# Kernel optimization log

Measured on AMD Instinct MI355X. Metric: run time of the kernel, lower is better.

## Reference

```python
import jax, jax.numpy as jnp
import numpy as np

T, H = 4096, 7168          # tokens, hidden size
Q_LORA, KV_LORA = 1536, 512
ROPE, NOPE, NH = 64, 128, 16
QK = NOPE + ROPE
MAXPOS, SLOTS = 8192, 16384
EPS = 1e-6


def _build_cos_sin_cache():
    # rotary cache layout used by the module: [max_pos, rope] = cos_half || sin_half
    half = ROPE // 2
    inv_freq = 1.0 / (10000.0 ** (np.arange(0, half, dtype=np.float32) / half))
    t = np.arange(MAXPOS, dtype=np.float32)
    freqs = np.outer(t, inv_freq)  # [MAXPOS, half]
    return jnp.asarray(np.concatenate([np.cos(freqs), np.sin(freqs)], axis=-1))


def setup_inputs() -> dict:
    key = jax.random.key(0)
    ks = jax.random.split(key, 8)
    return {
        "hidden_states": jax.random.normal(ks[0], (T, H), jnp.float32),
        "positions": jax.random.randint(ks[1], (T,), 0, MAXPOS, jnp.int32),
        "w_qkv_a": jax.random.normal(ks[2], (H, Q_LORA + KV_LORA + ROPE), jnp.float32) * 0.02,
        "q_a_ln_w": jnp.ones((Q_LORA,), jnp.float32),
        "w_q_b": jax.random.normal(ks[3], (Q_LORA, NH * QK), jnp.float32) * 0.02,
        "kv_a_ln_w": jnp.ones((KV_LORA,), jnp.float32),
        "w_kc": jax.random.normal(ks[4], (NH, NOPE, KV_LORA), jnp.float32) * 0.02,
        "cos_sin_cache": _build_cos_sin_cache(),
        "k_cache": jnp.zeros((SLOTS, KV_LORA), jnp.float32),
        "rope_cache": jnp.zeros((SLOTS, ROPE), jnp.float32),
        "slot_mapping": jnp.arange(T, dtype=jnp.int32),
    }


def _rms_norm(x, w, eps=EPS):
    return x * jax.lax.rsqrt(jnp.mean(x * x, axis=-1, keepdims=True) + eps) * w


def _interleave_rope(x, cos, sin):
    # npu_interleave_rope: de-interleave even/odd lanes into halves, then
    # apply neox-style rotation with full-dim (repeated) cos/sin.
    x1 = x[..., 0::2]
    x2 = x[..., 1::2]
    rot = jnp.concatenate([x1, x2], axis=-1)
    h = rot.shape[-1] // 2
    rot_half = jnp.concatenate([-rot[..., h:], rot[..., :h]], axis=-1)
    return rot * cos + rot_half * sin


def reference(hidden_states, positions, w_qkv_a, q_a_ln_w, w_q_b, kv_a_ln_w,
              w_kc, cos_sin_cache, k_cache, rope_cache, slot_mapping):
    # get_sin_cos: gather cache, chunk in halves, repeat each to full rope dim
    cs = cos_sin_cache[positions]                 # [T, ROPE]
    cos, sin = jnp.split(cs, 2, axis=-1)          # [T, ROPE/2] each
    cos = jnp.tile(cos, (1, 2))                   # [T, ROPE]
    sin = jnp.tile(sin, (1, 2))

    # fused qkv_a projection -> q low-rank + latent kv cache
    qkv = hidden_states @ w_qkv_a                 # [T, Q_LORA + KV_LORA + ROPE]
    q_low = qkv[:, :Q_LORA]
    latent = qkv[:, Q_LORA:]

    # q path: RMSNorm -> q_b projection -> per-head split
    q = _rms_norm(q_low, q_a_ln_w)
    q = (q @ w_q_b).reshape(-1, NH, QK)           # [T, NH, QK]
    q_nope, q_pe = q[..., :NOPE], q[..., NOPE:]

    # absorb: q_nope @ w_kc per head -> [T, NH, KV_LORA]
    q_nope = jnp.einsum("thn,hnk->thk", q_nope, w_kc)
    # interleaved rope on q_pe
    q_pe = _interleave_rope(q_pe, cos[:, None, :], sin[:, None, :])

    # kv path (npu_kv_rmsnorm_rope_cache): rmsnorm latent, rope the rope part,
    # scatter both into the paged caches at slot_mapping
    k_nope = _rms_norm(latent[:, :KV_LORA], kv_a_ln_w)     # [T, KV_LORA]
    k_rope = _interleave_rope(latent[:, KV_LORA:], cos, sin)  # [T, ROPE]
    k_cache = k_cache.at[slot_mapping].set(k_nope)
    rope_cache = rope_cache.at[slot_mapping].set(k_rope)

    q_out = jnp.concatenate([q_nope, q_pe], axis=-1)       # [T, NH, KV_LORA+ROPE]
    k_out = jnp.concatenate([k_nope, k_rope], axis=-1)     # [T, KV_LORA+ROPE]
    return q_out, k_out, k_cache, rope_cache
```

## Files before the change

kernel.cpp:

```cpp
#include <hip/hip_runtime.h>
#include <hip/hip_bf16.h>

typedef __bf16 bf16_t;
typedef __bf16 bf16x8 __attribute__((ext_vector_type(8)));
typedef float f32x4 __attribute__((ext_vector_type(4)));
typedef unsigned int uint;

#define T_TOK 4096
#define H_DIM 7168
#define QLORA 1536
#define KVLORA 512
#define ROPE_D 64
#define NOPE_D 128
#define NHEAD 16
#define NQKV 2112
#define NQB  3072
#define EPS_F 1e-6f


__global__ void cast_f32_bf16(const float* __restrict__ in, bf16_t* __restrict__ out, long n8)
{
    long stride = (long)gridDim.x * blockDim.x;
    for (long i = (long)blockIdx.x * blockDim.x + threadIdx.x; i < n8; i += stride) {
        const float4 a = ((const float4*)in)[i * 2];
        const float4 b = ((const float4*)in)[i * 2 + 1];
        bf16x8 v;
        v[0] = (bf16_t)a.x; v[1] = (bf16_t)a.y; v[2] = (bf16_t)a.z; v[3] = (bf16_t)a.w;
        v[4] = (bf16_t)b.x; v[5] = (bf16_t)b.y; v[6] = (bf16_t)b.z; v[7] = (bf16_t)b.w;
        ((bf16x8*)out)[i] = v;
    }
}

__global__ __launch_bounds__(256) void transpose_cast(const float* __restrict__ in,
                                                      bf16_t* __restrict__ out, int R, int C)
{
    __shared__ float tile[32][33];
    const int bx = blockIdx.x * 32;
    const int by = blockIdx.y * 32;
    const int tx = threadIdx.x & 31, ty = threadIdx.x >> 5;
    #pragma unroll
    for (int r = ty; r < 32; r += 8)
        tile[r][tx] = in[(long)(by + r) * C + bx + tx];
    __syncthreads();
    #pragma unroll
    for (int r = ty; r < 32; r += 8)
        out[(long)(bx + r) * R + by + tx] = (bf16_t)tile[tx][r];
}

__device__ inline float block_sum_256(float v)
{
    #pragma unroll
    for (int off = 32; off > 0; off >>= 1) v += __shfl_xor(v, off, 64);
    __shared__ float tmp[4];
    __syncthreads();
    if ((threadIdx.x & 63) == 0) tmp[threadIdx.x >> 6] = v;
    __syncthreads();
    return tmp[0] + tmp[1] + tmp[2] + tmp[3];
}

__global__ __launch_bounds__(256) void rmsq_kside_kernel(
    const float* __restrict__ qkv, const float* __restrict__ qkvB,
    const float* __restrict__ q_w, const float* __restrict__ kv_w,
    const float* __restrict__ cos_sin, const int* __restrict__ positions,
    const int* __restrict__ slot_map,
    bf16_t* __restrict__ q_a, float* __restrict__ k_out,
    float* __restrict__ kc_out, float* __restrict__ rc_out)
{
    const int t = blockIdx.x;
    const float* x = qkv + (long)t * NQKV;
    const float* xB = qkvB ? qkvB + (long)t * NQKV : nullptr;

    float loc[6];
    float ss = 0.f;
    #pragma unroll
    for (int i = 0; i < 6; i++) {
        int idx = threadIdx.x + 256 * i;
        float v = x[idx];
        if (xB) v += xB[idx];
        loc[i] = v; ss += v * v;
    }
    ss = block_sum_256(ss);
    const float scq = rsqrtf(ss / (float)QLORA + EPS_F);
    #pragma unroll
    for (int i = 0; i < 6; i++) {
        int idx = threadIdx.x + 256 * i;
        q_a[(long)t * QLORA + idx] = (bf16_t)(loc[i] * scq * q_w[idx]);
    }

    const float* lat = x + QLORA;
    const float* latB = xB ? xB + QLORA : nullptr;
    float v0 = lat[threadIdx.x];
    float v1 = lat[threadIdx.x + 256];
    if (latB) { v0 += latB[threadIdx.x]; v1 += latB[threadIdx.x + 256]; }
    float ssk = v0 * v0 + v1 * v1;
    ssk = block_sum_256(ssk);
    const float sck = rsqrtf(ssk / (float)KVLORA + EPS_F);
    const int slot = slot_map[t];
    const float a0 = v0 * sck * kv_w[threadIdx.x];
    const float a1 = v1 * sck * kv_w[threadIdx.x + 256];
    k_out[(long)t * 576 + threadIdx.x]        = a0;
    k_out[(long)t * 576 + 256 + threadIdx.x]  = a1;
    kc_out[(long)slot * KVLORA + threadIdx.x]       = a0;
    kc_out[(long)slot * KVLORA + 256 + threadIdx.x] = a1;
    if (threadIdx.x < 32) {
        const int j = threadIdx.x;
        const int pos = positions[t];
        const float c = cos_sin[pos * 64 + j];
        const float s = cos_sin[pos * 64 + 32 + j];
        float x1 = lat[KVLORA + 2 * j];
        float x2 = lat[KVLORA + 2 * j + 1];
        if (latB) { x1 += latB[KVLORA + 2 * j]; x2 += latB[KVLORA + 2 * j + 1]; }
        const float o1 = x1 * c - x2 * s;
        const float o2 = x2 * c + x1 * s;
        k_out[(long)t * 576 + 512 + j]      = o1;
        k_out[(long)t * 576 + 512 + 32 + j] = o2;
        rc_out[(long)slot * 64 + j]      = o1;
        rc_out[(long)slot * 64 + 32 + j] = o2;
    }
}

#define GBM 128
#define GBN 128
#define GBK 64

__global__ __launch_bounds__(512) void gemm_mfma(
    const bf16_t* __restrict__ A, int lda, long sA,
    const bf16_t* __restrict__ Bt, int ldb, long sB,
    float* __restrict__ C, int ldc, long sC,
    int K, int N)
{
    __shared__ bf16_t As[2][GBM * GBK];
    __shared__ bf16_t Bs[2][GBN * GBK];

    const int nwg = gridDim.x * gridDim.y;
    const int bid = blockIdx.y * gridDim.x + blockIdx.x;
    const int cpx = nwg >> 3;
    const int swz = (bid & 7) * cpx + (bid >> 3);
    const int bx = swz % gridDim.x;
    const int by = swz / gridDim.x;

    const int tid = threadIdx.x;
    const int lane = tid & 63;
    const int w = tid >> 6;
    const int wr = w >> 2, wc = w & 3;
    const int fr = lane & 15;
    const int kg = lane >> 4;

    const long brow = (long)by * GBM;
    const long bcol = (long)bx * GBN;

    const bf16_t* Ab = A + blockIdx.z * sA + brow * lda;
    const bf16_t* Bb = Bt + blockIdx.z * sB;
    float* Cb = C + blockIdx.z * sC + brow * ldc;

    const int srow = w * 16 + (lane >> 3);
    const int scol = (((lane & 7) ^ (lane >> 3)) * 8);

    const uint rd_sw = (uint)((kg * 16) ^ ((fr & 7) << 4));
    const uint a_base = (uint)(uintptr_t)(&As[0][0]) + (uint)((wr * 64 + fr) * 128) + rd_sw;
    const uint b_base = (uint)(uintptr_t)(&Bs[0][0]) + (uint)((wc * 32 + fr) * 128) + rd_sw;

    f32x4 acc[4][2] = {};

    const int nt = K / GBK;

    auto stage = [&](int buf, int k0) {
        #pragma unroll
        for (int it = 0; it < 2; it++) {
            const int r = srow + it * 8;
            __builtin_amdgcn_global_load_lds(
                (const __attribute__((address_space(1))) void*)(Ab + (long)r * lda + k0 + scol),
                (__attribute__((address_space(3))) void*)(&As[buf][(w * 16 + it * 8) * GBK]),
                16, 0, 0);
        }
        #pragma unroll
        for (int it = 0; it < 2; it++) {
            const int r = srow + it * 8;
            long bn = bcol + r; if (bn >= N) bn = N - 1;
            __builtin_amdgcn_global_load_lds(
                (const __attribute__((address_space(1))) void*)(Bb + bn * ldb + k0 + scol),
                (__attribute__((address_space(3))) void*)(&Bs[buf][(w * 16 + it * 8) * GBK]),
                16, 0, 0);
        }
    };

    stage(0, 0);
    asm volatile("s_waitcnt vmcnt(0)" ::: "memory");
    __builtin_amdgcn_s_barrier();

    int cur = 0;
    for (int t = 0; t < nt; ++t) {
        if (t + 1 < nt) stage(cur ^ 1, (t + 1) * GBK);

        const uint aa  = a_base + (uint)(cur * (GBM * GBK * 2));
        const uint bb  = b_base + (uint)(cur * (GBN * GBK * 2));
        const uint aaX = aa ^ 64u;
        const uint bbX = bb ^ 64u;
        bf16x8 a00, a01, a02, a03, a10, a11, a12, a13, b00, b01, b10, b11;
        asm volatile("ds_read_b128 %0, %1 offset:0"    : "=v"(a00) : "v"(aa));
        asm volatile("ds_read_b128 %0, %1 offset:2048" : "=v"(a01) : "v"(aa));
        asm volatile("ds_read_b128 %0, %1 offset:4096" : "=v"(a02) : "v"(aa));
        asm volatile("ds_read_b128 %0, %1 offset:6144" : "=v"(a03) : "v"(aa));
        asm volatile("ds_read_b128 %0, %1 offset:0"    : "=v"(a10) : "v"(aaX));
        asm volatile("ds_read_b128 %0, %1 offset:2048" : "=v"(a11) : "v"(aaX));
        asm volatile("ds_read_b128 %0, %1 offset:4096" : "=v"(a12) : "v"(aaX));
        asm volatile("ds_read_b128 %0, %1 offset:6144" : "=v"(a13) : "v"(aaX));
        asm volatile("ds_read_b128 %0, %1 offset:0"    : "=v"(b00) : "v"(bb));
        asm volatile("ds_read_b128 %0, %1 offset:2048" : "=v"(b01) : "v"(bb));
        asm volatile("ds_read_b128 %0, %1 offset:0"    : "=v"(b10) : "v"(bbX));
        asm volatile("ds_read_b128 %0, %1 offset:2048" : "=v"(b11) : "v"(bbX));
        asm volatile("s_waitcnt lgkmcnt(0)" ::: "memory");
        __builtin_amdgcn_sched_barrier(0);

        acc[0][0] = __builtin_amdgcn_mfma_f32_16x16x32_bf16(a00, b00, acc[0][0], 0, 0, 0);
        acc[0][1] = __builtin_amdgcn_mfma_f32_16x16x32_bf16(a00, b01, acc[0][1], 0, 0, 0);
        acc[1][0] = __builtin_amdgcn_mfma_f32_16x16x32_bf16(a01, b00, acc[1][0], 0, 0, 0);
        acc[1][1] = __builtin_amdgcn_mfma_f32_16x16x32_bf16(a01, b01, acc[1][1], 0, 0, 0);
        acc[2][0] = __builtin_amdgcn_mfma_f32_16x16x32_bf16(a02, b00, acc[2][0], 0, 0, 0);
        acc[2][1] = __builtin_amdgcn_mfma_f32_16x16x32_bf16(a02, b01, acc[2][1], 0, 0, 0);
        acc[3][0] = __builtin_amdgcn_mfma_f32_16x16x32_bf16(a03, b00, acc[3][0], 0, 0, 0);
        acc[3][1] = __builtin_amdgcn_mfma_f32_16x16x32_bf16(a03, b01, acc[3][1], 0, 0, 0);
        acc[0][0] = __builtin_amdgcn_mfma_f32_16x16x32_bf16(a10, b10, acc[0][0], 0, 0, 0);
        acc[0][1] = __builtin_amdgcn_mfma_f32_16x16x32_bf16(a10, b11, acc[0][1], 0, 0, 0);
        acc[1][0] = __builtin_amdgcn_mfma_f32_16x16x32_bf16(a11, b10, acc[1][0], 0, 0, 0);
        acc[1][1] = __builtin_amdgcn_mfma_f32_16x16x32_bf16(a11, b11, acc[1][1], 0, 0, 0);
        acc[2][0] = __builtin_amdgcn_mfma_f32_16x16x32_bf16(a12, b10, acc[2][0], 0, 0, 0);
        acc[2][1] = __builtin_amdgcn_mfma_f32_16x16x32_bf16(a12, b11, acc[2][1], 0, 0, 0);
        acc[3][0] = __builtin_amdgcn_mfma_f32_16x16x32_bf16(a13, b10, acc[3][0], 0, 0, 0);
        acc[3][1] = __builtin_amdgcn_mfma_f32_16x16x32_bf16(a13, b11, acc[3][1], 0, 0, 0);

        asm volatile("s_waitcnt vmcnt(0)" ::: "memory");
        __builtin_amdgcn_s_barrier();
        cur ^= 1;
    }

    #pragma unroll
    for (int i = 0; i < 4; i++) {
        #pragma unroll
        for (int j = 0; j < 2; j++) {
            const int row0 = wr * 64 + i * 16 + kg * 4;
            const long col = bcol + wc * 32 + j * 16 + fr;
            if (col < N) {
                #pragma unroll
                for (int r = 0; r < 4; r++)
                    Cb[(long)(row0 + r) * ldc + col] = acc[i][j][r];
            }
        }
    }
}

__global__ __launch_bounds__(512) void gemm2_fused(
    const bf16_t* __restrict__ A,
    const bf16_t* __restrict__ Bt,
    const float* __restrict__ cos_sin,
    const int* __restrict__ positions,
    bf16_t* __restrict__ q_nope,
    float* __restrict__ q_out)
{
    __shared__ bf16_t As[2][GBM * GBK];
    __shared__ bf16_t Bs[2][GBN * GBK];

    const int nwg = gridDim.x * gridDim.y;
    const int bid = blockIdx.y * gridDim.x + blockIdx.x;
    const int cpx = nwg >> 3;
    const int swz = (bid & 7) * cpx + (bid >> 3);
    const int bx = swz % gridDim.x;
    const int by = swz / gridDim.x;

    const int tid = threadIdx.x;
    const int lane = tid & 63;
    const int w = tid >> 6;
    const int wr = w >> 2, wc = w & 3;
    const int fr = lane & 15;
    const int kg = lane >> 4;

    const int brow = by * GBM;
    const int bcol = bx * GBN;

    const bf16_t* Ab = A + (long)brow * QLORA;
    const bf16_t* Bb = Bt + (long)bcol * QLORA;

    const int srow = w * 16 + (lane >> 3);
    const int scol = (((lane & 7) ^ (lane >> 3)) * 8);

    const uint rd_sw = (uint)((kg * 16) ^ ((fr & 7) << 4));
    const uint a_base = (uint)(uintptr_t)(&As[0][0]) + (uint)((wr * 64 + fr) * 128) + rd_sw;
    const uint b_base = (uint)(uintptr_t)(&Bs[0][0]) + (uint)((wc * 32 + fr) * 128) + rd_sw;

    f32x4 acc[4][2] = {};

    const int nt = QLORA / GBK;

    auto stage = [&](int buf, int k0) {
        #pragma unroll
        for (int it = 0; it < 2; it++) {
            const int r = srow + it * 8;
            __builtin_amdgcn_global_load_lds(
                (const __attribute__((address_space(1))) void*)(Ab + (long)r * QLORA + k0 + scol),
                (__attribute__((address_space(3))) void*)(&As[buf][(w * 16 + it * 8) * GBK]),
                16, 0, 0);
            __builtin_amdgcn_global_load_lds(
                (const __attribute__((address_space(1))) void*)(Bb + (long)r * QLORA + k0 + scol),
                (__attribute__((address_space(3))) void*)(&Bs[buf][(w * 16 + it * 8) * GBK]),
                16, 0, 0);
        }
    };

    stage(0, 0);
    asm volatile("s_waitcnt vmcnt(0)" ::: "memory");
    __builtin_amdgcn_s_barrier();

    int cur = 0;
    for (int t = 0; t < nt; ++t) {
        if (t + 1 < nt) stage(cur ^ 1, (t + 1) * GBK);

        const uint aa  = a_base + (uint)(cur * (GBM * GBK * 2));
        const uint bb  = b_base + (uint)(cur * (GBN * GBK * 2));
        const uint aaX = aa ^ 64u;
        const uint bbX = bb ^ 64u;
        bf16x8 a00, a01, a02, a03, a10, a11, a12, a13, b00, b01, b10, b11;
        asm volatile("ds_read_b128 %0, %1 offset:0"    : "=v"(a00) : "v"(aa));
        asm volatile("ds_read_b128 %0, %1 offset:2048" : "=v"(a01) : "v"(aa));
        asm volatile("ds_read_b128 %0, %1 offset:4096" : "=v"(a02) : "v"(aa));
        asm volatile("ds_read_b128 %0, %1 offset:6144" : "=v"(a03) : "v"(aa));
        asm volatile("ds_read_b128 %0, %1 offset:0"    : "=v"(a10) : "v"(aaX));
        asm volatile("ds_read_b128 %0, %1 offset:2048" : "=v"(a11) : "v"(aaX));
        asm volatile("ds_read_b128 %0, %1 offset:4096" : "=v"(a12) : "v"(aaX));
        asm volatile("ds_read_b128 %0, %1 offset:6144" : "=v"(a13) : "v"(aaX));
        asm volatile("ds_read_b128 %0, %1 offset:0"    : "=v"(b00) : "v"(bb));
        asm volatile("ds_read_b128 %0, %1 offset:2048" : "=v"(b01) : "v"(bb));
        asm volatile("ds_read_b128 %0, %1 offset:0"    : "=v"(b10) : "v"(bbX));
        asm volatile("ds_read_b128 %0, %1 offset:2048" : "=v"(b11) : "v"(bbX));
        asm volatile("s_waitcnt lgkmcnt(0)" ::: "memory");
        __builtin_amdgcn_sched_barrier(0);

        acc[0][0] = __builtin_amdgcn_mfma_f32_16x16x32_bf16(a00, b00, acc[0][0], 0, 0, 0);
        acc[0][1] = __builtin_amdgcn_mfma_f32_16x16x32_bf16(a00, b01, acc[0][1], 0, 0, 0);
        acc[1][0] = __builtin_amdgcn_mfma_f32_16x16x32_bf16(a01, b00, acc[1][0], 0, 0, 0);
        acc[1][1] = __builtin_amdgcn_mfma_f32_16x16x32_bf16(a01, b01, acc[1][1], 0, 0, 0);
        acc[2][0] = __builtin_amdgcn_mfma_f32_16x16x32_bf16(a02, b00, acc[2][0], 0, 0, 0);
        acc[2][1] = __builtin_amdgcn_mfma_f32_16x16x32_bf16(a02, b01, acc[2][1], 0, 0, 0);
        acc[3][0] = __builtin_amdgcn_mfma_f32_16x16x32_bf16(a03, b00, acc[3][0], 0, 0, 0);
        acc[3][1] = __builtin_amdgcn_mfma_f32_16x16x32_bf16(a03, b01, acc[3][1], 0, 0, 0);
        acc[0][0] = __builtin_amdgcn_mfma_f32_16x16x32_bf16(a10, b10, acc[0][0], 0, 0, 0);
        acc[0][1] = __builtin_amdgcn_mfma_f32_16x16x32_bf16(a10, b11, acc[0][1], 0, 0, 0);
        acc[1][0] = __builtin_amdgcn_mfma_f32_16x16x32_bf16(a11, b10, acc[1][0], 0, 0, 0);
        acc[1][1] = __builtin_amdgcn_mfma_f32_16x16x32_bf16(a11, b11, acc[1][1], 0, 0, 0);
        acc[2][0] = __builtin_amdgcn_mfma_f32_16x16x32_bf16(a12, b10, acc[2][0], 0, 0, 0);
        acc[2][1] = __builtin_amdgcn_mfma_f32_16x16x32_bf16(a12, b11, acc[2][1], 0, 0, 0);
        acc[3][0] = __builtin_amdgcn_mfma_f32_16x16x32_bf16(a13, b10, acc[3][0], 0, 0, 0);
        acc[3][1] = __builtin_amdgcn_mfma_f32_16x16x32_bf16(a13, b11, acc[3][1], 0, 0, 0);

        asm volatile("s_waitcnt vmcnt(0)" ::: "memory");
        __builtin_amdgcn_s_barrier();
        cur ^= 1;
    }

    #pragma unroll
    for (int i = 0; i < 4; i++) {
        #pragma unroll
        for (int j = 0; j < 2; j++) {
            const int row0 = wr * 64 + i * 16 + kg * 4;
            const int col  = bcol + wc * 32 + j * 16 + fr;
            const int h  = col / 192;
            const int jj = col - h * 192;
            if (jj < 128) {
                #pragma unroll
                for (int r = 0; r < 4; r++) {
                    const int t = brow + row0 + r;
                    q_nope[((long)h * T_TOK + t) * NOPE_D + jj] = (bf16_t)acc[i][j][r];
                }
            } else {
                const int idx = jj - 128;
                const int j2 = idx >> 1;
                const int odd = idx & 1;
                #pragma unroll
                for (int r = 0; r < 4; r++) {
                    const int t = brow + row0 + r;
                    const float v = acc[i][j][r];
                    const float p = __shfl_xor(v, 1, 64);
                    const int pos = positions[t];
                    const float c = cos_sin[pos * 64 + j2];
                    const float s = cos_sin[pos * 64 + 32 + j2];
                    const float o = odd ? (v * c + p * s) : (v * c - p * s);
                    q_out[(long)t * 9216 + h * 576 + 512 + (odd ? 32 : 0) + j2] = o;
                }
            }
        }
    }
}

__global__ __launch_bounds__(512) void gemm3_k128(
    const bf16_t* __restrict__ A,
    const bf16_t* __restrict__ Bt,
    float* __restrict__ C)
{
    __shared__ bf16_t As[2][GBM * GBK];
    __shared__ bf16_t Bs[2][GBN * GBK];

    const int nwg = gridDim.x * gridDim.y;
    const int bid = blockIdx.y * gridDim.x + blockIdx.x;
    const int cpx = nwg >> 3;
    const int swz = (bid & 7) * cpx + (bid >> 3);
    const int bx = swz % gridDim.x;
    const int by = swz / gridDim.x;

    const int tid = threadIdx.x;
    const int lane = tid & 63;
    const int w = tid >> 6;
    const int wr = w >> 2, wc = w & 3;
    const int fr = lane & 15;
    const int kg = lane >> 4;

    const long brow = (long)by * GBM;
    const long bcol = (long)bx * GBN;

    const bf16_t* Ab = A + (long)blockIdx.z * T_TOK * NOPE_D + brow * NOPE_D;
    const bf16_t* Bb = Bt + blockIdx.z * 128;
    float* Cb = C + blockIdx.z * 576 + brow * 9216;

    const int srow = w * 16 + (lane >> 3);
    const int scol = (((lane & 7) ^ (lane >> 3)) * 8);

    const uint rd_sw = (uint)((kg * 16) ^ ((fr & 7) << 4));

    #pragma unroll
    for (int kh = 0; kh < 2; kh++) {
        #pragma unroll
        for (int it = 0; it < 2; it++) {
            const int r = srow + it * 8;
            __builtin_amdgcn_global_load_lds(
                (const __attribute__((address_space(1))) void*)(Ab + (long)r * NOPE_D + kh * 64 + scol),
                (__attribute__((address_space(3))) void*)(&As[kh][(w * 16 + it * 8) * GBK]),
                16, 0, 0);
        }
        #pragma unroll
        for (int it = 0; it < 2; it++) {
            const int r = srow + it * 8;
            __builtin_amdgcn_global_load_lds(
                (const __attribute__((address_space(1))) void*)(Bb + (bcol + r) * 2048 + kh * 64 + scol),
                (__attribute__((address_space(3))) void*)(&Bs[kh][(w * 16 + it * 8) * GBK]),
                16, 0, 0);
        }
    }
    asm volatile("s_waitcnt vmcnt(0)" ::: "memory");
    __builtin_amdgcn_s_barrier();

    f32x4 acc[4][2] = {};

    #pragma unroll
    for (int kh = 0; kh < 2; kh++) {
        const uint aa  = (uint)(uintptr_t)(&As[kh][0]) + (uint)((wr * 64 + fr) * 128) + rd_sw;
        const uint bb  = (uint)(uintptr_t)(&Bs[kh][0]) + (uint)((wc * 32 + fr) * 128) + rd_sw;
        const uint aaX = aa ^ 64u;
        const uint bbX = bb ^ 64u;
        bf16x8 a00, a01, a02, a03, a10, a11, a12, a13, b00, b01, b10, b11;
        asm volatile("ds_read_b128 %0, %1 offset:0"    : "=v"(a00) : "v"(aa));
        asm volatile("ds_read_b128 %0, %1 offset:2048" : "=v"(a01) : "v"(aa));
        asm volatile("ds_read_b128 %0, %1 offset:4096" : "=v"(a02) : "v"(aa));
        asm volatile("ds_read_b128 %0, %1 offset:6144" : "=v"(a03) : "v"(aa));
        asm volatile("ds_read_b128 %0, %1 offset:0"    : "=v"(a10) : "v"(aaX));
        asm volatile("ds_read_b128 %0, %1 offset:2048" : "=v"(a11) : "v"(aaX));
        asm volatile("ds_read_b128 %0, %1 offset:4096" : "=v"(a12) : "v"(aaX));
        asm volatile("ds_read_b128 %0, %1 offset:6144" : "=v"(a13) : "v"(aaX));
        asm volatile("ds_read_b128 %0, %1 offset:0"    : "=v"(b00) : "v"(bb));
        asm volatile("ds_read_b128 %0, %1 offset:2048" : "=v"(b01) : "v"(bb));
        asm volatile("ds_read_b128 %0, %1 offset:0"    : "=v"(b10) : "v"(bbX));
        asm volatile("ds_read_b128 %0, %1 offset:2048" : "=v"(b11) : "v"(bbX));
        asm volatile("s_waitcnt lgkmcnt(0)" ::: "memory");
        __builtin_amdgcn_sched_barrier(0);

        acc[0][0] = __builtin_amdgcn_mfma_f32_16x16x32_bf16(a00, b00, acc[0][0], 0, 0, 0);
        acc[0][1] = __builtin_amdgcn_mfma_f32_16x16x32_bf16(a00, b01, acc[0][1], 0, 0, 0);
        acc[1][0] = __builtin_amdgcn_mfma_f32_16x16x32_bf16(a01, b00, acc[1][0], 0, 0, 0);
        acc[1][1] = __builtin_amdgcn_mfma_f32_16x16x32_bf16(a01, b01, acc[1][1], 0, 0, 0);
        acc[2][0] = __builtin_amdgcn_mfma_f32_16x16x32_bf16(a02, b00, acc[2][0], 0, 0, 0);
        acc[2][1] = __builtin_amdgcn_mfma_f32_16x16x32_bf16(a02, b01, acc[2][1], 0, 0, 0);
        acc[3][0] = __builtin_amdgcn_mfma_f32_16x16x32_bf16(a03, b00, acc[3][0], 0, 0, 0);
        acc[3][1] = __builtin_amdgcn_mfma_f32_16x16x32_bf16(a03, b01, acc[3][1], 0, 0, 0);
        acc[0][0] = __builtin_amdgcn_mfma_f32_16x16x32_bf16(a10, b10, acc[0][0], 0, 0, 0);
        acc[0][1] = __builtin_amdgcn_mfma_f32_16x16x32_bf16(a10, b11, acc[0][1], 0, 0, 0);
        acc[1][0] = __builtin_amdgcn_mfma_f32_16x16x32_bf16(a11, b10, acc[1][0], 0, 0, 0);
        acc[1][1] = __builtin_amdgcn_mfma_f32_16x16x32_bf16(a11, b11, acc[1][1], 0, 0, 0);
        acc[2][0] = __builtin_amdgcn_mfma_f32_16x16x32_bf16(a12, b10, acc[2][0], 0, 0, 0);
        acc[2][1] = __builtin_amdgcn_mfma_f32_16x16x32_bf16(a12, b11, acc[2][1], 0, 0, 0);
        acc[3][0] = __builtin_amdgcn_mfma_f32_16x16x32_bf16(a13, b10, acc[3][0], 0, 0, 0);
        acc[3][1] = __builtin_amdgcn_mfma_f32_16x16x32_bf16(a13, b11, acc[3][1], 0, 0, 0);
    }

    #pragma unroll
    for (int i = 0; i < 4; i++) {
        #pragma unroll
        for (int j = 0; j < 2; j++) {
            const int row0 = wr * 64 + i * 16 + kg * 4;
            const long col = bcol + wc * 32 + j * 16 + fr;
            #pragma unroll
            for (int r = 0; r < 4; r++)
                Cb[(long)(row0 + r) * 9216 + col] = acc[i][j][r];
        }
    }
}


extern "C" void kernel_launch(void* const* d_in, const int* in_sizes, int n_in,
                              void* d_out, int out_size, void* d_ws, size_t ws_size,
                              hipStream_t stream)
{
    const float* hs       = (const float*)d_in[0];
    const int*   positions= (const int*)d_in[1];
    const float* w_qkv_a  = (const float*)d_in[2];
    const float* q_a_ln_w = (const float*)d_in[3];
    const float* w_q_b    = (const float*)d_in[4];
    const float* kv_a_ln_w= (const float*)d_in[5];
    const float* w_kc     = (const float*)d_in[6];
    const float* cos_sin  = (const float*)d_in[7];
    const float* k_cache_in  = (const float*)d_in[8];
    const float* rope_cache_in = (const float*)d_in[9];
    const int*   slot_map = (const int*)d_in[10];

    float* out   = (float*)d_out;
    float* q_out = out;
    float* k_out = out + 37748736;
    float* kc_out = out + 40108032;
    float* rc_out = out + 48496640;

    char* ws = (char*)d_ws;
    bf16_t* hs_bf  = (bf16_t*)(ws + 0);
    bf16_t* wqkvaT = (bf16_t*)(ws + 58720256);
    bf16_t* wqbT   = (bf16_t*)(ws + 88997888);
    bf16_t* wkcT   = (bf16_t*)(ws + 98435072);
    float*  qkv0   = (float*)(ws + 100532224);

    const bool splitk = ws_size >= (size_t)169738240;

    float*  qkv1;
    bf16_t* q_a;
    bf16_t* q_nope;
    if (splitk) {
        qkv1   = (float*)(ws + 135135232);
        q_a    = (bf16_t*)(ws + 0);
        q_nope = (bf16_t*)(ws + 135135232);
    } else {
        qkv1   = nullptr;
        q_a    = (bf16_t*)(ws + 135135232);
        q_nope = (bf16_t*)(ws + 100532224);
    }

    hipMemcpyAsync(kc_out, k_cache_in, (size_t)16384 * 512 * 4, hipMemcpyDeviceToDevice, stream);
    hipMemcpyAsync(rc_out, rope_cache_in, (size_t)16384 * 64 * 4, hipMemcpyDeviceToDevice, stream);

    cast_f32_bf16<<<2048, 256, 0, stream>>>(hs, hs_bf, (long)T_TOK * H_DIM / 8);
    transpose_cast<<<dim3(NQKV / 32, H_DIM / 32), 256, 0, stream>>>(w_qkv_a, wqkvaT, H_DIM, NQKV);
    transpose_cast<<<dim3(NQB / 32, QLORA / 32), 256, 0, stream>>>(w_q_b, wqbT, QLORA, NQB);
    transpose_cast<<<dim3(512 / 32, 2048 / 32), 256, 0, stream>>>(w_kc, wkcT, 2048, 512);

    if (splitk) {
        gemm_mfma<<<dim3((NQKV + GBN - 1) / GBN, T_TOK / GBM, 2), 512, 0, stream>>>(
            hs_bf, H_DIM, 3584, wqkvaT, H_DIM, 3584,
            qkv0, NQKV, (long)T_TOK * NQKV, 3584, NQKV);
    } else {
        gemm_mfma<<<dim3((NQKV + GBN - 1) / GBN, T_TOK / GBM, 1), 512, 0, stream>>>(
            hs_bf, H_DIM, 0, wqkvaT, H_DIM, 0, qkv0, NQKV, 0, H_DIM, NQKV);
    }

    rmsq_kside_kernel<<<T_TOK, 256, 0, stream>>>(qkv0, qkv1, q_a_ln_w, kv_a_ln_w,
                                                 cos_sin, positions, slot_map,
                                                 q_a, k_out, kc_out, rc_out);

    gemm2_fused<<<dim3(NQB / GBN, T_TOK / GBM), 512, 0, stream>>>(
        q_a, wqbT, cos_sin, positions, q_nope, q_out);

    gemm3_k128<<<dim3(KVLORA / GBN, T_TOK / GBM, NHEAD), 512, 0, stream>>>(
        q_nope, wkcT, q_out);
}
```

Baseline: 367.8 us.

## Vectorize weight transpose with 64x64 tiles and allow four-way split-K

The weight transpose-cast kernel now uses 64x64 shared tiles with float4 loads and 4-wide bf16 stores, which cuts per-element memory transactions. The first GEMM can split K four ways when the workspace is large enough, adding parallelism. The rmsnorm kernel sums up to four partial fp32 outputs. The four-way split costs extra workspace and more partial-sum traffic.

```diff
diff --git a/kernel.cpp b/kernel.cpp
--- a/kernel.cpp
+++ b/kernel.cpp
@@ -2,6 +2,7 @@
 #include <hip/hip_bf16.h>
 
 typedef __bf16 bf16_t;
+typedef __bf16 bf16x4 __attribute__((ext_vector_type(4)));
 typedef __bf16 bf16x8 __attribute__((ext_vector_type(8)));
 typedef float f32x4 __attribute__((ext_vector_type(4)));
 typedef unsigned int uint;
@@ -31,20 +32,31 @@
     }
 }
 
-__global__ __launch_bounds__(256) void transpose_cast(const float* __restrict__ in,
-                                                      bf16_t* __restrict__ out, int R, int C)
-{
-    __shared__ float tile[32][33];
-    const int bx = blockIdx.x * 32;
-    const int by = blockIdx.y * 32;
-    const int tx = threadIdx.x & 31, ty = threadIdx.x >> 5;
-    #pragma unroll
-    for (int r = ty; r < 32; r += 8)
-        tile[r][tx] = in[(long)(by + r) * C + bx + tx];
+__global__ __launch_bounds__(256) void transpose_cast64(const float* __restrict__ in,
+                                                        bf16_t* __restrict__ out, int R, int C)
+{
+    __shared__ float tile[64][65];
+    const int bx = blockIdx.x * 64;
+    const int by = blockIdx.y * 64;
+    const int tx = threadIdx.x & 15, ty = threadIdx.x >> 4;
+    #pragma unroll
+    for (int i = 0; i < 4; i++) {
+        const int r = ty + 16 * i;
+        const float4 v = *(const float4*)&in[(long)(by + r) * C + bx + tx * 4];
+        tile[r][tx * 4 + 0] = v.x; tile[r][tx * 4 + 1] = v.y;
+        tile[r][tx * 4 + 2] = v.z; tile[r][tx * 4 + 3] = v.w;
+    }
     __syncthreads();
     #pragma unroll
-    for (int r = ty; r < 32; r += 8)
-        out[(long)(bx + r) * R + by + tx] = (bf16_t)tile[tx][r];
+    for (int i = 0; i < 4; i++) {
+        const int cc = ty + 16 * i;
+        bf16x4 o;
+        o[0] = (bf16_t)tile[tx * 4 + 0][cc];
+        o[1] = (bf16_t)tile[tx * 4 + 1][cc];
+        o[2] = (bf16_t)tile[tx * 4 + 2][cc];
+        o[3] = (bf16_t)tile[tx * 4 + 3][cc];
+        *(bf16x4*)&out[(long)(bx + cc) * R + by + tx * 4] = o;
+    }
 }
 
 __device__ inline float block_sum_256(float v)
@@ -59,7 +71,8 @@
 }
 
 __global__ __launch_bounds__(256) void rmsq_kside_kernel(
-    const float* __restrict__ qkv, const float* __restrict__ qkvB,
+    const float* __restrict__ qkv, const float* __restrict__ qB,
+    const float* __restrict__ qC, const float* __restrict__ qD,
     const float* __restrict__ q_w, const float* __restrict__ kv_w,
     const float* __restrict__ cos_sin, const int* __restrict__ positions,
     const int* __restrict__ slot_map,
@@ -67,8 +80,11 @@
     float* __restrict__ kc_out, float* __restrict__ rc_out)
 {
     const int t = blockIdx.x;
-    const float* x = qkv + (long)t * NQKV;
-    const float* xB = qkvB ? qkvB + (long)t * NQKV : nullptr;
+    const long base = (long)t * NQKV;
+    const float* x = qkv + base;
+    const float* xB = qB ? qB + base : nullptr;
+    const float* xC = qC ? qC + base : nullptr;
+    const float* xD = qD ? qD + base : nullptr;
 
     float loc[6];
     float ss = 0.f;
@@ -77,6 +93,8 @@
         int idx = threadIdx.x + 256 * i;
         float v = x[idx];
         if (xB) v += xB[idx];
+        if (xC) v += xC[idx];
+        if (xD) v += xD[idx];
         loc[i] = v; ss += v * v;
     }
     ss = block_sum_256(ss);
@@ -87,11 +105,11 @@
         q_a[(long)t * QLORA + idx] = (bf16_t)(loc[i] * scq * q_w[idx]);
     }
 
-    const float* lat = x + QLORA;
-    const float* latB = xB ? xB + QLORA : nullptr;
-    float v0 = lat[threadIdx.x];
-    float v1 = lat[threadIdx.x + 256];
-    if (latB) { v0 += latB[threadIdx.x]; v1 += latB[threadIdx.x + 256]; }
+    float v0 = x[QLORA + threadIdx.x];
+    float v1 = x[QLORA + threadIdx.x + 256];
+    if (xB) { v0 += xB[QLORA + threadIdx.x]; v1 += xB[QLORA + threadIdx.x + 256]; }
+    if (xC) { v0 += xC[QLORA + threadIdx.x]; v1 += xC[QLORA + threadIdx.x + 256]; }
+    if (xD) { v0 += xD[QLORA + threadIdx.x]; v1 += xD[QLORA + threadIdx.x + 256]; }
     float ssk = v0 * v0 + v1 * v1;
     ssk = block_sum_256(ssk);
     const float sck = rsqrtf(ssk / (float)KVLORA + EPS_F);
@@ -107,9 +125,11 @@
         const int pos = positions[t];
         const float c = cos_sin[pos * 64 + j];
         const float s = cos_sin[pos * 64 + 32 + j];
-        float x1 = lat[KVLORA + 2 * j];
-        float x2 = lat[KVLORA + 2 * j + 1];
-        if (latB) { x1 += latB[KVLORA + 2 * j]; x2 += latB[KVLORA + 2 * j + 1]; }
+        float x1 = x[QLORA + KVLORA + 2 * j];
+        float x2 = x[QLORA + KVLORA + 2 * j + 1];
+        if (xB) { x1 += xB[QLORA + KVLORA + 2 * j]; x2 += xB[QLORA + KVLORA + 2 * j + 1]; }
+        if (xC) { x1 += xC[QLORA + KVLORA + 2 * j]; x2 += xC[QLORA + KVLORA + 2 * j + 1]; }
+        if (xD) { x1 += xD[QLORA + KVLORA + 2 * j]; x2 += xD[QLORA + KVLORA + 2 * j + 1]; }
         const float o1 = x1 * c - x2 * s;
         const float o2 = x2 * c + x1 * s;
         k_out[(long)t * 576 + 512 + j]      = o1;
@@ -531,17 +551,22 @@
     bf16_t* wkcT   = (bf16_t*)(ws + 98435072);
     float*  qkv0   = (float*)(ws + 100532224);
 
-    const bool splitk = ws_size >= (size_t)169738240;
-
-    float*  qkv1;
+    int splitk = 1;
+    if (ws_size >= (size_t)238944256) splitk = 4;
+    else if (ws_size >= (size_t)169738240) splitk = 2;
+
+    float* qkv1 = nullptr; float* qkv2 = nullptr; float* qkv3 = nullptr;
     bf16_t* q_a;
     bf16_t* q_nope;
-    if (splitk) {
+    if (splitk >= 2) {
         qkv1   = (float*)(ws + 135135232);
         q_a    = (bf16_t*)(ws + 0);
         q_nope = (bf16_t*)(ws + 135135232);
+        if (splitk == 4) {
+            qkv2 = (float*)(ws + 169738240);
+            qkv3 = (float*)(ws + 204341248);
+        }
     } else {
-        qkv1   = nullptr;
         q_a    = (bf16_t*)(ws + 135135232);
         q_nope = (bf16_t*)(ws + 100532224);
     }
@@ -550,20 +575,19 @@
     hipMemcpyAsync(rc_out, rope_cache_in, (size_t)16384 * 64 * 4, hipMemcpyDeviceToDevice, stream);
 
     cast_f32_bf16<<<2048, 256, 0, stream>>>(hs, hs_bf, (long)T_TOK * H_DIM / 8);
-    transpose_cast<<<dim3(NQKV / 32, H_DIM / 32), 256, 0, stream>>>(w_qkv_a, wqkvaT, H_DIM, NQKV);
-    transpose_cast<<<dim3(NQB / 32, QLORA / 32), 256, 0, stream>>>(w_q_b, wqbT, QLORA, NQB);
-    transpose_cast<<<dim3(512 / 32, 2048 / 32), 256, 0, stream>>>(w_kc, wkcT, 2048, 512);
-
-    if (splitk) {
-        gemm_mfma<<<dim3((NQKV + GBN - 1) / GBN, T_TOK / GBM, 2), 512, 0, stream>>>(
-            hs_bf, H_DIM, 3584, wqkvaT, H_DIM, 3584,
-            qkv0, NQKV, (long)T_TOK * NQKV, 3584, NQKV);
-    } else {
-        gemm_mfma<<<dim3((NQKV + GBN - 1) / GBN, T_TOK / GBM, 1), 512, 0, stream>>>(
-            hs_bf, H_DIM, 0, wqkvaT, H_DIM, 0, qkv0, NQKV, 0, H_DIM, NQKV);
-    }
-
-    rmsq_kside_kernel<<<T_TOK, 256, 0, stream>>>(qkv0, qkv1, q_a_ln_w, kv_a_ln_w,
+    transpose_cast64<<<dim3(NQKV / 64, H_DIM / 64), 256, 0, stream>>>(w_qkv_a, wqkvaT, H_DIM, NQKV);
+    transpose_cast64<<<dim3(NQB / 64, QLORA / 64), 256, 0, stream>>>(w_q_b, wqbT, QLORA, NQB);
+    transpose_cast64<<<dim3(512 / 64, 2048 / 64), 256, 0, stream>>>(w_kc, wkcT, 2048, 512);
+
+    {
+        const int kslice = H_DIM / splitk;
+        gemm_mfma<<<dim3((NQKV + GBN - 1) / GBN, T_TOK / GBM, splitk), 512, 0, stream>>>(
+            hs_bf, H_DIM, kslice, wqkvaT, H_DIM, kslice,
+            qkv0, NQKV, (long)T_TOK * NQKV, kslice, NQKV);
+    }
+
+    rmsq_kside_kernel<<<T_TOK, 256, 0, stream>>>(qkv0, qkv1, qkv2, qkv3,
+                                                 q_a_ln_w, kv_a_ln_w,
                                                  cos_sin, positions, slot_map,
                                                  q_a, k_out, kc_out, rc_out);
 
```

New measurement: 373.5 us. No clear change (+1.5%).
